# Kernel optimization log

Measured on AMD Instinct MI355X. Metric: run time of the kernel, lower is better.

The kernel has to match this reference:

```python
import jax, jax.numpy as jnp
import numpy as np

B, S, E, H = 1, 2048, 4096, 32
D = E // H
MAX_POS = 2048
NEG_MASK = -66504.0
SCALE = float(np.sqrt(D))


def _rope(x, position_ids):
    # x: [B, S, H, D]; GPT-NeoX style rotate-half rotary embedding
    half = D // 2
    inv_freq = 1.0 / (10000.0 ** (jnp.arange(0, half, dtype=jnp.float32) * 2.0 / D))  # [D/2]
    ang = position_ids.astype(jnp.float32)[:, None] * inv_freq[None, :]               # [S, D/2]
    cos = jnp.cos(ang)[None, :, None, :]
    sin = jnp.sin(ang)[None, :, None, :]
    x1, x2 = x[..., :half], x[..., half:]
    return jnp.concatenate([x1 * cos - x2 * sin, x2 * cos + x1 * sin], axis=-1)


def setup_inputs() -> dict:
    key = jax.random.key(0)
    ks = jax.random.split(key, 9)
    s = 0.02
    return {
        "hidden_states": jax.random.normal(ks[0], (B, S, E), jnp.float32),
        "wq": jax.random.normal(ks[1], (E, E), jnp.float32) * s,
        "bq": jnp.zeros((E,), jnp.float32),
        "wk": jax.random.normal(ks[2], (E, E), jnp.float32) * s,
        "bk": jnp.zeros((E,), jnp.float32),
        "wv": jax.random.normal(ks[3], (E, E), jnp.float32) * s,
        "bv": jnp.zeros((E,), jnp.float32),
        "wo": jax.random.normal(ks[4], (E, E), jnp.float32) * s,
        "bo": jnp.zeros((E,), jnp.float32),
        "position_ids": jnp.arange(S, dtype=jnp.int32),
    }


def reference(hidden_states, wq, bq, wk, bk, wv, bv, wo, bo, position_ids):
    # QKV projections (nn.Linear: x @ W.T + b)
    q = hidden_states @ wq.T + bq
    k = hidden_states @ wk.T + bk
    v = hidden_states @ wv.T + bv
    # [B, S, H, D]
    q = q.reshape(B, S, H, D)
    k = k.reshape(B, S, H, D)
    v = v.reshape(B, S, H, D)
    # rotary embedding on key and query
    q = _rope(q, position_ids)
    k = _rope(k, position_ids)
    # [B, H, S, D]
    q = q.transpose(0, 2, 1, 3)
    k = k.transpose(0, 2, 1, 3)
    v = v.transpose(0, 2, 1, 3)
    # attention scores; causal mask added BEFORE dividing by scale (faithful to source)
    scores = jnp.einsum("bhqd,bhkd->bhqk", q, k)
    causal = (1.0 - jnp.tril(jnp.ones((S, S), jnp.float32))) * NEG_MASK  # [S, S]
    scores = (scores + causal[None, None]) / SCALE
    attn = jax.nn.softmax(scores.astype(jnp.float32), axis=-1).astype(q.dtype)
    ctx = jnp.einsum("bhqk,bhkd->bhqd", attn, v)
    ctx = ctx.transpose(0, 2, 1, 3).reshape(B, S, E)
    return ctx @ wo.T + bo
```

## Files before the change

### kernel.cpp

```cpp
#include <hip/hip_runtime.h>
#include <hip/hip_bf16.h>

constexpr int SEQ = 2048;
constexpr int EMB = 4096;
constexpr int NH  = 32;
constexpr int HD  = 128;
constexpr int HALF = 64;

typedef __bf16 bf16x8 __attribute__((ext_vector_type(8)));
typedef float  f32x4  __attribute__((ext_vector_type(4)));
using u16 = unsigned short;
typedef u16 ushort8 __attribute__((ext_vector_type(8)));
typedef u16 u16x4 __attribute__((ext_vector_type(4)));

__device__ inline float bf2f(u16 u) {
  union { unsigned int i; float f; } v; v.i = ((unsigned int)u) << 16; return v.f;
}
__device__ inline u16 f2bf(float f) {
  union { __bf16 b; u16 u; } v; v.b = (__bf16)f; return v.u;
}

#define GLL16(gp, lp) __builtin_amdgcn_global_load_lds( \
    (const __attribute__((address_space(1))) void*)(gp), \
    (__attribute__((address_space(3))) void*)(lp), 16, 0, 0)

__global__ void k_f32_to_bf16(const float* __restrict__ in, u16* __restrict__ out, int n) {
  int i = (blockIdx.x * blockDim.x + threadIdx.x) * 8;
  if (i >= n) return;
  f32x4 a = *(const f32x4*)(in + i);
  f32x4 b = *(const f32x4*)(in + i + 4);
  ushort8 o;
  o[0] = f2bf(a[0]); o[1] = f2bf(a[1]); o[2] = f2bf(a[2]); o[3] = f2bf(a[3]);
  o[4] = f2bf(b[0]); o[5] = f2bf(b[1]); o[6] = f2bf(b[2]); o[7] = f2bf(b[3]);
  *(ushort8*)(out + i) = o;
}

__global__ void k_w3_to_bf16(const float* __restrict__ w0, const float* __restrict__ w1,
                             const float* __restrict__ w2, u16* __restrict__ out) {
  size_t i = ((size_t)blockIdx.x * blockDim.x + threadIdx.x) * 8;
  int seg = (int)(i >> 24);
  size_t off = i & ((1u << 24) - 1);
  const float* src = (seg == 0) ? w0 : (seg == 1) ? w1 : w2;
  f32x4 a = *(const f32x4*)(src + off);
  f32x4 b = *(const f32x4*)(src + off + 4);
  ushort8 o;
  o[0] = f2bf(a[0]); o[1] = f2bf(a[1]); o[2] = f2bf(a[2]); o[3] = f2bf(a[3]);
  o[4] = f2bf(b[0]); o[5] = f2bf(b[1]); o[6] = f2bf(b[2]); o[7] = f2bf(b[3]);
  *(ushort8*)(out + i) = o;
}

__global__ void k_rope_table(const int* __restrict__ pos, float* __restrict__ tab) {
  int idx = blockIdx.x * blockDim.x + threadIdx.x;
  if (idx >= SEQ * HALF) return;
  int s = idx >> 6, d = idx & 63;
  double invf = pow(10000.0, -(double)d / 64.0);
  double ang = (double)pos[s] * invf;
  tab[idx * 2]     = (float)cos(ang);
  tab[idx * 2 + 1] = (float)sin(ang);
}

__global__ void k_rope(u16* __restrict__ X, const float* __restrict__ tab, float scale) {
  int idx = blockIdx.x * blockDim.x + threadIdx.x;
  if (idx >= SEQ * NH * HALF) return;
  int d = idx & 63;
  int h = (idx >> 6) & 31;
  int s = idx >> 11;
  u16* p = X + (size_t)s * EMB + h * HD + d;
  float x1 = bf2f(p[0]), x2 = bf2f(p[HALF]);
  float c  = tab[(s * HALF + d) * 2];
  float sn = tab[(s * HALF + d) * 2 + 1];
  p[0]    = f2bf((x1 * c - x2 * sn) * scale);
  p[HALF] = f2bf((x2 * c + x1 * sn) * scale);
}

template<int TBM>
__global__ __launch_bounds__(512, 1) void k_qkv4(
    const u16* __restrict__ Ag, const u16* __restrict__ Wg,
    const float* __restrict__ b0, const float* __restrict__ b1, const float* __restrict__ b2,
    void* __restrict__ C0, void* __restrict__ C1, void* __restrict__ C2,
    int M, int N, int K, int mode)
{
  constexpr int LDA = TBM / 128;
  constexpr int LPT = LDA + 2;
  constexpr int MA  = TBM / 32;
  __shared__ alignas(16) u16 As[4][TBM * 32];
  __shared__ alignas(16) u16 Bs[4][256 * 32];

  int tid = threadIdx.x;
  int lane = tid & 63, wid = tid >> 6;
  int wm = wid >> 2, wn = wid & 3;
  int l15 = lane & 15, lhi = lane >> 4;

  int NBY = M / TBM, NBX = N >> 8;
  int wg = blockIdx.x;
  int xcd = wg & 7, sgl = wg >> 3;
  int by = sgl % NBY, bxl = sgl / NBY;
  int bx = xcd * (NBX >> 3) + bxl;
  int m0 = by * TBM, n0 = bx * 256;

  auto stageA = [&](int b, int k0) {
#pragma unroll
    for (int ld = 0; ld < LDA; ld++) {
      int idx = ld * 512 + tid;
      int row = idx >> 2, pb = idx & 3;
      int kb = (pb - row - (row >> 2)) & 3;
      GLL16(Ag + (size_t)(m0 + row) * K + k0 + kb * 8, &As[b][idx * 8]);
    }
  };
  auto stageB = [&](int b, int k0) {
#pragma unroll
    for (int ld = 0; ld < 2; ld++) {
      int idx = ld * 512 + tid;
      int row = idx >> 2, pb = idx & 3;
      int kb = (pb - row - (row >> 2)) & 3;
      GLL16(Wg + (size_t)(n0 + row) * K + k0 + kb * 8, &Bs[b][idx * 8]);
    }
  };

  f32x4 acc[MA][4] = {};
  int KT = K >> 5;

  stageA(0, 0);  stageB(0, 0);
  stageA(1, 32); stageB(1, 32);
  stageA(2, 64); stageB(2, 64);

  for (int t = 0; t < KT; t++) {
    if (t < KT - 2)       asm volatile("s_waitcnt vmcnt(%0)" :: "n"(2 * LPT) : "memory");
    else if (t == KT - 2) asm volatile("s_waitcnt vmcnt(%0)" :: "n"(LPT) : "memory");
    else                  asm volatile("s_waitcnt vmcnt(0)" ::: "memory");
    __builtin_amdgcn_s_barrier();
    __builtin_amdgcn_sched_barrier(0);

    const u16* as = &As[t & 3][0];
    const u16* bs = &Bs[t & 3][0];
    bool st = (t + 3) < KT;
    int sb = (t + 3) & 3, sk = (t + 3) << 5;

    bf16x8 bfr[4], afA[4];
#pragma unroll
    for (int q = 0; q < 4; q++) {
      int row = wn * 64 + q * 16 + l15;
      bfr[q] = *(const bf16x8*)&bs[row * 32 + ((lhi + row + (row >> 2)) & 3) * 8];
    }
#pragma unroll
    for (int p = 0; p < MA / 2; p++) {
      int row = wm * (TBM / 2) + p * 16 + l15;
      afA[p] = *(const bf16x8*)&as[row * 32 + ((lhi + row + (row >> 2)) & 3) * 8];
    }
    if (st) stageA(sb, sk);
    __builtin_amdgcn_s_setprio(1);
#pragma unroll
    for (int p = 0; p < MA / 2; p++)
#pragma unroll
      for (int q = 0; q < 4; q++)
        acc[p][q] = __builtin_amdgcn_mfma_f32_16x16x32_bf16(afA[p], bfr[q], acc[p][q], 0, 0, 0);
    __builtin_amdgcn_s_setprio(0);

    bf16x8 afB[MA / 2];
#pragma unroll
    for (int p = 0; p < MA / 2; p++) {
      int row = wm * (TBM / 2) + (MA / 2) * 16 + p * 16 + l15;
      afB[p] = *(const bf16x8*)&as[row * 32 + ((lhi + row + (row >> 2)) & 3) * 8];
    }
    if (st) stageB(sb, sk);
    __builtin_amdgcn_s_setprio(1);
#pragma unroll
    for (int p = 0; p < MA / 2; p++)
#pragma unroll
      for (int q = 0; q < 4; q++)
        acc[MA / 2 + p][q] = __builtin_amdgcn_mfma_f32_16x16x32_bf16(afB[p], bfr[q], acc[MA / 2 + p][q], 0, 0, 0);
    __builtin_amdgcn_s_setprio(0);
  }

  int mode_l = mode, Nn = N, n_base = n0;
  const float* bias = b0;
  void* Cout = C0;
  if (mode == 3) {
    int seg = n0 >> 12;
    Nn = EMB; n_base = n0 & 4095;
    if (seg == 0)      { bias = b0; Cout = C0; mode_l = 0; }
    else if (seg == 1) { bias = b1; Cout = C1; mode_l = 0; }
    else               { bias = b2; Cout = C2; mode_l = 2; }
  }

#pragma unroll
  for (int p = 0; p < MA; p++) {
    int m = m0 + wm * (TBM / 2) + p * 16 + lhi * 4;
#pragma unroll
    for (int q = 0; q < 4; q++) {
      int n = n_base + wn * 64 + q * 16 + l15;
      float bs2 = bias[n];
      if (mode_l == 2) {
        u16x4 pk;
#pragma unroll
        for (int r = 0; r < 4; r++) pk[r] = f2bf(acc[p][q][r] + bs2);
        *(u16x4*)&((u16*)Cout)[(size_t)n * M + m] = pk;
      } else if (mode_l == 1) {
#pragma unroll
        for (int r = 0; r < 4; r++)
          ((float*)Cout)[(size_t)(m + r) * Nn + n] = acc[p][q][r] + bs2;
      } else {
#pragma unroll
        for (int r = 0; r < 4; r++)
          ((u16*)Cout)[(size_t)(m + r) * Nn + n] = f2bf(acc[p][q][r] + bs2);
      }
    }
  }
}

constexpr int QB = 128, KVB = 64;

__global__ __launch_bounds__(512) void k_flash(
    const u16* __restrict__ Q, const u16* __restrict__ K, const u16* __restrict__ VT,
    u16* __restrict__ ctx)
{
  __shared__ alignas(16) u16 Ks[2][KVB * 128];
  __shared__ alignas(16) u16 Vt[2][HD * 64];
  __shared__ alignas(16) u16 Pl[8][16 * 64];

  int tid = threadIdx.x, lane = tid & 63, wid = tid >> 6;
  int l15 = lane & 15, lhi = lane >> 4;
  int h = blockIdx.y;

  auto stage = [&](int buf, int t2) {
    int kv = t2 * KVB;
#pragma unroll
    for (int it = 0; it < 2; it++) {
      int chunk = tid + it * 512;
      int r = chunk >> 4, bp = chunk & 15;
      GLL16(K + (size_t)(kv + r) * EMB + h * HD + (((bp - r) & 15) << 3), &Ks[buf][chunk * 8]);
    }
#pragma unroll
    for (int it = 0; it < 2; it++) {
      int chunk = tid + it * 512;
      int d = chunk >> 3, bp = chunk & 7;
      GLL16(VT + (size_t)(h * HD + d) * SEQ + kv + (((bp - d) & 7) << 3), &Vt[buf][chunk * 8]);
    }
  };

  for (int pi = 0; pi < 2; pi++) {
    int qb = pi ? (int)blockIdx.x : 15 - (int)blockIdx.x;
    int q0 = qb * QB;
    int qw = q0 + wid * 16;

    bf16x8 qf[4];
#pragma unroll
    for (int kc = 0; kc < 4; kc++)
      qf[kc] = *(const bf16x8*)&Q[(size_t)(qw + l15) * EMB + h * HD + kc * 32 + lhi * 8];

    f32x4 O[8] = {};
    float mrow[4], lrow[4];
#pragma unroll
    for (int r = 0; r < 4; r++) { mrow[r] = -3.0e38f; lrow[r] = 0.f; }

    int nt = 2 * (qb + 1);
    __syncthreads();
    stage(0, 0);
    for (int t = 0; t < nt; t++) {
      __syncthreads();
      if (t + 1 < nt) stage((t + 1) & 1, t + 1);

      int kv0 = t * KVB;
      if (kv0 > qw + 15) continue;

      const u16* ks = Ks[t & 1];
      const u16* vt = Vt[t & 1];
      float p[4][4];
      bool need_mask = (kv0 + KVB - 1) > qw;
#pragma unroll
      for (int c = 0; c < 4; c++) {
        f32x4 s = {};
        int r0 = c * 16 + l15;
#pragma unroll
        for (int kc = 0; kc < 4; kc++) {
          bf16x8 kf = *(const bf16x8*)&ks[r0 * 128 + (((kc * 4 + lhi) + r0) & 15) * 8];
          s = __builtin_amdgcn_mfma_f32_16x16x32_bf16(qf[kc], kf, s, 0, 0, 0);
        }
#pragma unroll
        for (int r = 0; r < 4; r++) {
          float sv = s[r];
          if (need_mask) {
            int qg = qw + lhi * 4 + r;
            int kg = kv0 + c * 16 + l15;
            if (kg > qg) sv = -3.0e38f;
          }
          p[c][r] = sv;
        }
      }
      float fscale[4];
#pragma unroll
      for (int r = 0; r < 4; r++) {
        float m = fmaxf(fmaxf(p[0][r], p[1][r]), fmaxf(p[2][r], p[3][r]));
#pragma unroll
        for (int x = 1; x < 16; x <<= 1) m = fmaxf(m, __shfl_xor(m, x, 64));
        float mnew = fmaxf(mrow[r], m);
        fscale[r] = __expf(mrow[r] - mnew);
        mrow[r] = mnew;
      }
#pragma unroll
      for (int c = 0; c < 4; c++)
#pragma unroll
        for (int r = 0; r < 4; r++)
          p[c][r] = __expf(p[c][r] - mrow[r]);
#pragma unroll
      for (int r = 0; r < 4; r++) {
        float s = p[0][r] + p[1][r] + p[2][r] + p[3][r];
#pragma unroll
        for (int x = 1; x < 16; x <<= 1) s += __shfl_xor(s, x, 64);
        lrow[r] = lrow[r] * fscale[r] + s;
      }
#pragma unroll
      for (int d = 0; d < 8; d++)
#pragma unroll
        for (int r = 0; r < 4; r++)
          O[d][r] *= fscale[r];
#pragma unroll
      for (int c = 0; c < 4; c++) {
        int kb = c * 2 + (l15 >> 3), klo = l15 & 7;
#pragma unroll
        for (int r = 0; r < 4; r++) {
          int q = lhi * 4 + r;
          Pl[wid][q * 64 + ((kb + (q >> 1)) & 7) * 8 + klo] = f2bf(p[c][r]);
        }
      }
#pragma unroll
      for (int ks2 = 0; ks2 < 2; ks2++) {
        int kb = ks2 * 4 + lhi;
        bf16x8 pf = *(const bf16x8*)&Pl[wid][l15 * 64 + ((kb + (l15 >> 1)) & 7) * 8];
#pragma unroll
        for (int ds = 0; ds < 8; ds++) {
          int d = ds * 16 + l15;
          bf16x8 vf = *(const bf16x8*)&vt[d * 64 + ((kb + d) & 7) * 8];
          O[ds] = __builtin_amdgcn_mfma_f32_16x16x32_bf16(pf, vf, O[ds], 0, 0, 0);
        }
      }
    }

#pragma unroll
    for (int r = 0; r < 4; r++) {
      float inv = 1.f / lrow[r];
      int qg = q0 + wid * 16 + lhi * 4 + r;
#pragma unroll
      for (int ds = 0; ds < 8; ds++)
        ctx[(size_t)qg * EMB + h * HD + ds * 16 + l15] = f2bf(O[ds][r] * inv);
    }
  }
}

extern "C" void kernel_launch(void* const* d_in, const int* in_sizes, int n_in,
                              void* d_out, int out_size, void* d_ws, size_t ws_size,
                              hipStream_t stream) {
  const float* hs = (const float*)d_in[0];
  const float* wq = (const float*)d_in[1];
  const float* bq = (const float*)d_in[2];
  const float* wk = (const float*)d_in[3];
  const float* bk = (const float*)d_in[4];
  const float* wv = (const float*)d_in[5];
  const float* bv = (const float*)d_in[6];
  const float* wo = (const float*)d_in[7];
  const float* bo = (const float*)d_in[8];
  const int*  pos = (const int*)d_in[9];

  const size_t SE = (size_t)SEQ * EMB;
  const size_t EE = (size_t)EMB * EMB;
  const float qscale = 1.0f / 11.313708498984761f;

  char* ws = (char*)d_ws;
  size_t off = 0;
  auto alloc = [&](size_t b) { size_t o = off; off += (b + 255) & ~(size_t)255; return o; };

  size_t need_fused = ((SE * 2 + 255) & ~255ULL) + ((EE * 6 + 255) & ~255ULL) +
                      3 * ((SE * 2 + 255) & ~255ULL) + ((size_t)SEQ * HALF * 8 + 255);
  bool fused = ws_size >= need_fused + 4096;

  u16*  hsb = (u16*)(ws + alloc(SE * 2));
  u16*  wb  = (u16*)(ws + alloc(fused ? EE * 6 : EE * 2));
  u16*  Qb  = (u16*)(ws + alloc(SE * 2));
  u16*  Kb  = (u16*)(ws + alloc(SE * 2));
  u16*  VTb = (u16*)(ws + alloc(SE * 2));
  float* tab = (float*)(ws + alloc((size_t)SEQ * HALF * 2 * 4));
  u16*  ctxb = hsb;

  dim3 cb(256);
  k_f32_to_bf16<<<dim3(SE / 2048), cb, 0, stream>>>(hs, hsb, (int)SE);
  k_rope_table<<<dim3(SEQ * HALF / 256), cb, 0, stream>>>(pos, tab);

  if (fused) {
    k_w3_to_bf16<<<dim3(3 * EE / 2048), cb, 0, stream>>>(wq, wk, wv, wb);
    k_qkv4<256><<<dim3(384), dim3(512), 0, stream>>>(
        hsb, wb, bq, bk, bv, (void*)Qb, (void*)Kb, (void*)VTb, SEQ, 3 * EMB, EMB, 3);
  } else {
    k_f32_to_bf16<<<dim3(EE / 2048), cb, 0, stream>>>(wq, wb, (int)EE);
    k_qkv4<256><<<dim3(128), dim3(512), 0, stream>>>(
        hsb, wb, bq, bq, bq, (void*)Qb, nullptr, nullptr, SEQ, EMB, EMB, 0);
    k_f32_to_bf16<<<dim3(EE / 2048), cb, 0, stream>>>(wk, wb, (int)EE);
    k_qkv4<256><<<dim3(128), dim3(512), 0, stream>>>(
        hsb, wb, bk, bk, bk, (void*)Kb, nullptr, nullptr, SEQ, EMB, EMB, 0);
    k_f32_to_bf16<<<dim3(EE / 2048), cb, 0, stream>>>(wv, wb, (int)EE);
    k_qkv4<256><<<dim3(128), dim3(512), 0, stream>>>(
        hsb, wb, bv, bv, bv, (void*)VTb, nullptr, nullptr, SEQ, EMB, EMB, 2);
  }

  k_rope<<<dim3(SEQ * NH * HALF / 256), cb, 0, stream>>>(Qb, tab, qscale);
  k_rope<<<dim3(SEQ * NH * HALF / 256), cb, 0, stream>>>(Kb, tab, 1.0f);

  k_flash<<<dim3(8, NH), dim3(512), 0, stream>>>(Qb, Kb, VTb, ctxb);

  k_f32_to_bf16<<<dim3(EE / 2048), cb, 0, stream>>>(wo, wb, (int)EE);
  k_qkv4<128><<<dim3(256), dim3(512), 0, stream>>>(
      ctxb, wb, bo, bo, bo, d_out, nullptr, nullptr, SEQ, EMB, EMB, 1);
}
```

Measured before the change: 501.6 us.

## Restructure GEMM to BK=64 double-buffered pipeline with 8-way LDS swizzle

```diff
diff --git a/kernel.cpp b/kernel.cpp
--- a/kernel.cpp
+++ b/kernel.cpp
@@ -74,17 +74,17 @@
 }
 
 template<int TBM>
-__global__ __launch_bounds__(512, 1) void k_qkv4(
+__global__ __launch_bounds__(512, 1) void k_gemm64(
     const u16* __restrict__ Ag, const u16* __restrict__ Wg,
     const float* __restrict__ b0, const float* __restrict__ b1, const float* __restrict__ b2,
     void* __restrict__ C0, void* __restrict__ C1, void* __restrict__ C2,
     int M, int N, int K, int mode)
 {
-  constexpr int LDA = TBM / 128;
-  constexpr int LPT = LDA + 2;
-  constexpr int MA  = TBM / 32;
-  __shared__ alignas(16) u16 As[4][TBM * 32];
-  __shared__ alignas(16) u16 Bs[4][256 * 32];
+  constexpr int MA = TBM / 32;
+  constexpr int MH = MA / 4;
+  constexpr int LA = TBM / 64;
+  __shared__ alignas(16) u16 As[2][TBM * 64];
+  __shared__ alignas(16) u16 Bs[2][256 * 64];
 
   int tid = threadIdx.x;
   int lane = tid & 63, wid = tid >> 6;
@@ -98,78 +98,64 @@
   int bx = xcd * (NBX >> 3) + bxl;
   int m0 = by * TBM, n0 = bx * 256;
 
-  auto stageA = [&](int b, int k0) {
-#pragma unroll
-    for (int ld = 0; ld < LDA; ld++) {
+  auto stage = [&](int b, int k0) {
+#pragma unroll
+    for (int ld = 0; ld < LA; ld++) {
       int idx = ld * 512 + tid;
-      int row = idx >> 2, pb = idx & 3;
-      int kb = (pb - row - (row >> 2)) & 3;
+      int row = idx >> 3, pb = idx & 7;
+      int kb = (pb - row) & 7;
       GLL16(Ag + (size_t)(m0 + row) * K + k0 + kb * 8, &As[b][idx * 8]);
     }
+#pragma unroll
+    for (int ld = 0; ld < 4; ld++) {
+      int idx = ld * 512 + tid;
+      int row = idx >> 3, pb = idx & 7;
+      int kb = (pb - row) & 7;
+      GLL16(Wg + (size_t)(n0 + row) * K + k0 + kb * 8, &Bs[b][idx * 8]);
+    }
   };
-  auto stageB = [&](int b, int k0) {
-#pragma unroll
-    for (int ld = 0; ld < 2; ld++) {
-      int idx = ld * 512 + tid;
-      int row = idx >> 2, pb = idx & 3;
-      int kb = (pb - row - (row >> 2)) & 3;
-      GLL16(Wg + (size_t)(n0 + row) * K + k0 + kb * 8, &Bs[b][idx * 8]);
-    }
-  };
 
   f32x4 acc[MA][4] = {};
-  int KT = K >> 5;
-
-  stageA(0, 0);  stageB(0, 0);
-  stageA(1, 32); stageB(1, 32);
-  stageA(2, 64); stageB(2, 64);
-
+  int KT = K >> 6;
+
+  stage(0, 0);
   for (int t = 0; t < KT; t++) {
-    if (t < KT - 2)       asm volatile("s_waitcnt vmcnt(%0)" :: "n"(2 * LPT) : "memory");
-    else if (t == KT - 2) asm volatile("s_waitcnt vmcnt(%0)" :: "n"(LPT) : "memory");
-    else                  asm volatile("s_waitcnt vmcnt(0)" ::: "memory");
+    asm volatile("s_waitcnt vmcnt(0)" ::: "memory");
     __builtin_amdgcn_s_barrier();
     __builtin_amdgcn_sched_barrier(0);
-
-    const u16* as = &As[t & 3][0];
-    const u16* bs = &Bs[t & 3][0];
-    bool st = (t + 3) < KT;
-    int sb = (t + 3) & 3, sk = (t + 3) << 5;
-
-    bf16x8 bfr[4], afA[4];
-#pragma unroll
-    for (int q = 0; q < 4; q++) {
-      int row = wn * 64 + q * 16 + l15;
-      bfr[q] = *(const bf16x8*)&bs[row * 32 + ((lhi + row + (row >> 2)) & 3) * 8];
-    }
-#pragma unroll
-    for (int p = 0; p < MA / 2; p++) {
-      int row = wm * (TBM / 2) + p * 16 + l15;
-      afA[p] = *(const bf16x8*)&as[row * 32 + ((lhi + row + (row >> 2)) & 3) * 8];
-    }
-    if (st) stageA(sb, sk);
-    __builtin_amdgcn_s_setprio(1);
-#pragma unroll
-    for (int p = 0; p < MA / 2; p++)
-#pragma unroll
-      for (int q = 0; q < 4; q++)
-        acc[p][q] = __builtin_amdgcn_mfma_f32_16x16x32_bf16(afA[p], bfr[q], acc[p][q], 0, 0, 0);
-    __builtin_amdgcn_s_setprio(0);
-
-    bf16x8 afB[MA / 2];
-#pragma unroll
-    for (int p = 0; p < MA / 2; p++) {
-      int row = wm * (TBM / 2) + (MA / 2) * 16 + p * 16 + l15;
-      afB[p] = *(const bf16x8*)&as[row * 32 + ((lhi + row + (row >> 2)) & 3) * 8];
-    }
-    if (st) stageB(sb, sk);
-    __builtin_amdgcn_s_setprio(1);
-#pragma unroll
-    for (int p = 0; p < MA / 2; p++)
-#pragma unroll
-      for (int q = 0; q < 4; q++)
-        acc[MA / 2 + p][q] = __builtin_amdgcn_mfma_f32_16x16x32_bf16(afB[p], bfr[q], acc[MA / 2 + p][q], 0, 0, 0);
-    __builtin_amdgcn_s_setprio(0);
+    if (t + 1 < KT) {
+      stage((t + 1) & 1, (t + 1) << 6);
+      __builtin_amdgcn_sched_barrier(0);
+    }
+
+    const u16* as = &As[t & 1][0];
+    const u16* bs = &Bs[t & 1][0];
+#pragma unroll
+    for (int ks = 0; ks < 2; ks++) {
+      bf16x8 bfr[4];
+#pragma unroll
+      for (int q = 0; q < 4; q++) {
+        int row = wn * 64 + q * 16 + l15;
+        bfr[q] = *(const bf16x8*)&bs[row * 64 + (((ks * 4 + lhi) + row) & 7) * 8];
+      }
+#pragma unroll
+      for (int mh = 0; mh < MH; mh++) {
+        bf16x8 af[4];
+#pragma unroll
+        for (int p = 0; p < 4; p++) {
+          int row = wm * (TBM / 2) + mh * 64 + p * 16 + l15;
+          af[p] = *(const bf16x8*)&as[row * 64 + (((ks * 4 + lhi) + row) & 7) * 8];
+        }
+        __builtin_amdgcn_s_setprio(1);
+#pragma unroll
+        for (int p = 0; p < 4; p++)
+#pragma unroll
+          for (int q = 0; q < 4; q++)
+            acc[mh * 4 + p][q] =
+                __builtin_amdgcn_mfma_f32_16x16x32_bf16(af[p], bfr[q], acc[mh * 4 + p][q], 0, 0, 0);
+        __builtin_amdgcn_s_setprio(0);
+      }
+    }
   }
 
   int mode_l = mode, Nn = N, n_base = n0;
@@ -387,17 +373,17 @@
 
   if (fused) {
     k_w3_to_bf16<<<dim3(3 * EE / 2048), cb, 0, stream>>>(wq, wk, wv, wb);
-    k_qkv4<256><<<dim3(384), dim3(512), 0, stream>>>(
+    k_gemm64<256><<<dim3(384), dim3(512), 0, stream>>>(
         hsb, wb, bq, bk, bv, (void*)Qb, (void*)Kb, (void*)VTb, SEQ, 3 * EMB, EMB, 3);
   } else {
     k_f32_to_bf16<<<dim3(EE / 2048), cb, 0, stream>>>(wq, wb, (int)EE);
-    k_qkv4<256><<<dim3(128), dim3(512), 0, stream>>>(
+    k_gemm64<128><<<dim3(256), dim3(512), 0, stream>>>(
         hsb, wb, bq, bq, bq, (void*)Qb, nullptr, nullptr, SEQ, EMB, EMB, 0);
     k_f32_to_bf16<<<dim3(EE / 2048), cb, 0, stream>>>(wk, wb, (int)EE);
-    k_qkv4<256><<<dim3(128), dim3(512), 0, stream>>>(
+    k_gemm64<128><<<dim3(256), dim3(512), 0, stream>>>(
         hsb, wb, bk, bk, bk, (void*)Kb, nullptr, nullptr, SEQ, EMB, EMB, 0);
     k_f32_to_bf16<<<dim3(EE / 2048), cb, 0, stream>>>(wv, wb, (int)EE);
-    k_qkv4<256><<<dim3(128), dim3(512), 0, stream>>>(
+    k_gemm64<128><<<dim3(256), dim3(512), 0, stream>>>(
         hsb, wb, bv, bv, bv, (void*)VTb, nullptr, nullptr, SEQ, EMB, EMB, 2);
   }
 
@@ -407,6 +393,6 @@
   k_flash<<<dim3(8, NH), dim3(512), 0, stream>>>(Qb, Kb, VTb, ctxb);
 
   k_f32_to_bf16<<<dim3(EE / 2048), cb, 0, stream>>>(wo, wb, (int)EE);
-  k_qkv4<128><<<dim3(256), dim3(512), 0, stream>>>(
+  k_gemm64<128><<<dim3(256), dim3(512), 0, stream>>>(
       ctxb, wb, bo, bo, bo, d_out, nullptr, nullptr, SEQ, EMB, EMB, 1);
 }
```

Result: slower. 539.1 us (+7.5%).
